# Optimization experiments

Measured on AMD Instinct MI355X. Metric: run time of the kernel, lower is better.

Reference implementation:

```python
import jax, jax.numpy as jnp
import numpy as np

TEMPERATURE = 32.0  # sqrt(d_model=1024)

def setup_inputs() -> dict:
    key = jax.random.key(0)
    kq, kk, kv = jax.random.split(key, 3)
    B, H, S, D = 2, 16, 2048, 64
    q = jax.random.normal(kq, (B, H, S, D), dtype=jnp.float32)
    k = jax.random.normal(kk, (B, H, S, D), dtype=jnp.float32)
    v = jax.random.normal(kv, (B, H, S, D), dtype=jnp.float32)
    mask = jnp.ones((B, 1, 1, S), dtype=jnp.int32)  # key-padding mask, 1 = keep
    return {"q": q, "k": k, "v": v, "mask": mask}

def reference(q, k, v, mask):
    # scores: [B,H,S,S]
    scores = jnp.einsum('bhqd,bhkd->bhqk', q / TEMPERATURE, k)
    scores = jnp.where(mask == 0, jnp.float32(-1e9), scores)
    attention = jax.nn.softmax(scores, axis=-1)
    # dropout is identity at inference (module's nn.Dropout in eval mode)
    output = jnp.einsum('bhqk,bhkd->bhqd', attention, v)
    return (output, attention)
```

## Files before the change

### kernel.cpp

```cpp
#include <hip/hip_runtime.h>
#include <hip/hip_bf16.h>


#define S_LEN 2048
#define D_DIM 64
#define BM 64
#define BN 64
#define NT (S_LEN / BN)
#define LDP 72
#define PSTR 136
#define BH_N 32

typedef __attribute__((ext_vector_type(8))) short bf16x8;
typedef __attribute__((ext_vector_type(4))) float f32x4;

__device__ __forceinline__ unsigned pack_bf16(float a, float b) {
    union { __hip_bfloat162 h; unsigned u; } cv;
    cv.h = __float22bfloat162_rn(make_float2(a, b));
    return cv.u;
}
__device__ __forceinline__ unsigned short bf1(float x) {
    union { __hip_bfloat16 h; unsigned short u; } cv;
    cv.h = __float2bfloat16(x);
    return cv.u;
}
__device__ __forceinline__ float bf2f(unsigned bits) {
    return __uint_as_float(bits);
}

__global__ __launch_bounds__(256)
void conv_k(const float* __restrict__ Kg, unsigned short* __restrict__ Kw) {
    size_t i = (size_t)(blockIdx.x * 256 + threadIdx.x) * 8;
    const float4 v0 = *(const float4*)(Kg + i);
    const float4 v1 = *(const float4*)(Kg + i + 4);
    uint4 o;
    o.x = pack_bf16(v0.x, v0.y);
    o.y = pack_bf16(v0.z, v0.w);
    o.z = pack_bf16(v1.x, v1.y);
    o.w = pack_bf16(v1.z, v1.w);
    *(uint4*)(Kw + i) = o;
}

__global__ __launch_bounds__(256)
void conv_vt(const float* __restrict__ Vg, unsigned short* __restrict__ Vtw) {
    const int bh = blockIdx.y;
    const int d  = threadIdx.x & 63;
    const int kq = threadIdx.x >> 6;
    const int key0 = blockIdx.x * 32 + kq * 8;
    const float* Vb = Vg + ((size_t)bh * S_LEN + key0) * D_DIM + d;
    float f[8];
    #pragma unroll
    for (int i = 0; i < 8; ++i) f[i] = Vb[i * D_DIM];
    uint4 o;
    o.x = pack_bf16(f[0], f[1]);
    o.y = pack_bf16(f[2], f[3]);
    o.z = pack_bf16(f[4], f[5]);
    o.w = pack_bf16(f[6], f[7]);
    *(uint4*)(Vtw + ((size_t)bh * D_DIM + d) * S_LEN + key0) = o;
}

template <int PRE>
__global__ __launch_bounds__(256, 4)
void attn_kernel(const float* __restrict__ Qg, const float* __restrict__ Kg,
                 const float* __restrict__ Vg, const int* __restrict__ Mg,
                 const unsigned short* __restrict__ Kw,
                 const unsigned short* __restrict__ Vtw,
                 float* __restrict__ Og, float* __restrict__ Ag) {
    __shared__ unsigned short Ks[BN * LDP];
    __shared__ unsigned short QV[D_DIM * LDP];
    __shared__ unsigned short Pb[BM * PSTR];
    __shared__ int maskS[BN];

    const int tid  = threadIdx.x;
    const int w    = tid >> 6;
    const int lane = tid & 63;
    const int l15  = lane & 15;
    const int quad = lane >> 4;

    const int qt = blockIdx.x;
    const int bh = blockIdx.y;
    const int b  = bh >> 4;
    const int q0 = qt * BM;
    const int qrow = w * 16 + l15;

    const float* Qb = Qg + ((size_t)bh * S_LEN + q0) * D_DIM;
    const int*   Mb = Mg + (size_t)b * S_LEN;
    float* Ob = Og + ((size_t)bh * S_LEN + q0) * D_DIM;
    float* Ab = Ag + ((size_t)bh * S_LEN + q0) * (size_t)S_LEN;

    {
        const float sc = 0.04508422f;
        #pragma unroll
        for (int i = 0; i < 4; ++i) {
            int f = tid + i * 256;
            int row = f >> 4, c4 = f & 15;
            const float4 v = *(const float4*)(Qb + row * D_DIM + c4 * 4);
            *(uint2*)(&QV[row * LDP + c4 * 4]) =
                make_uint2(pack_bf16(v.x * sc, v.y * sc), pack_bf16(v.z * sc, v.w * sc));
        }
    }
    __syncthreads();

    bf16x8 aq[2];
    #pragma unroll
    for (int ks = 0; ks < 2; ++ks)
        aq[ks] = *(const bf16x8*)(&QV[qrow * LDP + ks * 32 + quad * 8]);

    auto stage_k = [&](int key0) {
        if constexpr (PRE) {
            const unsigned short* Kt = Kw + (size_t)bh * S_LEN * D_DIM + (size_t)key0 * D_DIM;
            #pragma unroll
            for (int i = 0; i < 2; ++i) {
                int idx = tid + i * 256;
                int row = idx >> 3, c = idx & 7;
                uint4 vv = *(const uint4*)(Kt + row * D_DIM + c * 8);
                *(uint4*)(&Ks[row * LDP + c * 8]) = vv;
            }
        } else {
            const float* Kb = Kg + ((size_t)bh * S_LEN + key0) * D_DIM;
            #pragma unroll
            for (int i = 0; i < 4; ++i) {
                int f = tid + i * 256;
                int row = f >> 4, c4 = f & 15;
                const float4 v = *(const float4*)(Kb + row * D_DIM + c4 * 4);
                *(uint2*)(&Ks[row * LDP + c4 * 4]) =
                    make_uint2(pack_bf16(v.x, v.y), pack_bf16(v.z, v.w));
            }
        }
    };
    auto stage_v = [&](int key0) {
        if constexpr (PRE) {
            const unsigned short* Vt = Vtw + (size_t)bh * D_DIM * S_LEN + key0;
            #pragma unroll
            for (int i = 0; i < 2; ++i) {
                int idx = tid + i * 256;
                int d = idx >> 3, c = idx & 7;
                uint4 vv = *(const uint4*)(Vt + (size_t)d * S_LEN + c * 8);
                *(uint4*)(&QV[d * LDP + c * 8]) = vv;
            }
        } else {
            int key = tid & 63, g = tid >> 6;
            #pragma unroll
            for (int i = 0; i < 4; ++i) {
                int d0 = (g * 4 + i) * 4;
                const float4 v = *(const float4*)(Vg + ((size_t)bh * S_LEN + key0 + key) * D_DIM + d0);
                QV[(d0 + 0) * LDP + key] = bf1(v.x);
                QV[(d0 + 1) * LDP + key] = bf1(v.y);
                QV[(d0 + 2) * LDP + key] = bf1(v.z);
                QV[(d0 + 3) * LDP + key] = bf1(v.w);
            }
        }
    };

    float lsum = 0.f;

    for (int kt = 0; kt < NT; ++kt) {
        const int key0 = kt * BN;
        stage_k(key0);
        if (tid < BN) maskS[tid] = Mb[key0 + tid];
        __syncthreads();

        #pragma unroll
        for (int cb = 0; cb < 4; ++cb) {
            f32x4 acc = {0.f, 0.f, 0.f, 0.f};
            #pragma unroll
            for (int ks = 0; ks < 2; ++ks) {
                bf16x8 bk = *(const bf16x8*)(&Ks[(cb * 16 + l15) * LDP + ks * 32 + quad * 8]);
                acc = __builtin_amdgcn_mfma_f32_16x16x32_bf16(bk, aq[ks], acc, 0, 0, 0);
            }
            const int4 m4 = *(const int4*)(&maskS[cb * 16 + quad * 4]);
            float e0 = m4.x ? __builtin_exp2f(acc[0]) : 0.f;
            float e1 = m4.y ? __builtin_exp2f(acc[1]) : 0.f;
            float e2 = m4.z ? __builtin_exp2f(acc[2]) : 0.f;
            float e3 = m4.w ? __builtin_exp2f(acc[3]) : 0.f;
            lsum += (e0 + e1) + (e2 + e3);
        }
        __syncthreads();
    }

    lsum += __shfl_xor(lsum, 16);
    lsum += __shfl_xor(lsum, 32);
    const float linv = 1.0f / lsum;

    f32x4 oacc[4];
    #pragma unroll
    for (int db = 0; db < 4; ++db) oacc[db] = (f32x4){0.f, 0.f, 0.f, 0.f};

    for (int kt2 = 0; kt2 < NT / 2; ++kt2) {
        #pragma unroll
        for (int half = 0; half < 2; ++half) {
            const int key0 = (kt2 * 2 + half) * BN;
            stage_k(key0);
            stage_v(key0);
            if (tid < BN) maskS[tid] = Mb[key0 + tid];
            __syncthreads();

            #pragma unroll
            for (int cb = 0; cb < 4; ++cb) {
                f32x4 acc = {0.f, 0.f, 0.f, 0.f};
                #pragma unroll
                for (int ks = 0; ks < 2; ++ks) {
                    bf16x8 bk = *(const bf16x8*)(&Ks[(cb * 16 + l15) * LDP + ks * 32 + quad * 8]);
                    acc = __builtin_amdgcn_mfma_f32_16x16x32_bf16(bk, aq[ks], acc, 0, 0, 0);
                }
                const int4 m4 = *(const int4*)(&maskS[cb * 16 + quad * 4]);
                float p0 = (m4.x ? __builtin_exp2f(acc[0]) : 0.f) * linv;
                float p1 = (m4.y ? __builtin_exp2f(acc[1]) : 0.f) * linv;
                float p2 = (m4.z ? __builtin_exp2f(acc[2]) : 0.f) * linv;
                float p3 = (m4.w ? __builtin_exp2f(acc[3]) : 0.f) * linv;
                *(uint2*)(&Pb[qrow * PSTR + half * 64 + cb * 16 + quad * 4]) =
                    make_uint2(pack_bf16(p0, p1), pack_bf16(p2, p3));
            }

            #pragma unroll
            for (int ks2 = 0; ks2 < 2; ++ks2) {
                bf16x8 ap = *(const bf16x8*)(&Pb[qrow * PSTR + half * 64 + ks2 * 32 + quad * 8]);
                #pragma unroll
                for (int db = 0; db < 4; ++db) {
                    bf16x8 bv = *(const bf16x8*)(&QV[(db * 16 + l15) * LDP + ks2 * 32 + quad * 8]);
                    oacc[db] = __builtin_amdgcn_mfma_f32_16x16x32_bf16(bv, ap, oacc[db], 0, 0, 0);
                }
            }
            __syncthreads();
        }

        const int key00 = kt2 * 2 * BN;
        #pragma unroll
        for (int i = 0; i < 8; ++i) {
            int idx = tid + i * 256;
            int row = idx >> 5, c4 = idx & 31;
            uint2 pu = *(const uint2*)(&Pb[row * PSTR + c4 * 4]);
            f32x4 t;
            t[0] = bf2f(pu.x << 16); t[1] = bf2f(pu.x & 0xffff0000u);
            t[2] = bf2f(pu.y << 16); t[3] = bf2f(pu.y & 0xffff0000u);
            __builtin_nontemporal_store(
                t, (f32x4*)(Ab + (size_t)row * S_LEN + key00 + c4 * 4));
        }
    }

    #pragma unroll
    for (int db = 0; db < 4; ++db) {
        f32x4 o4 = oacc[db];
        __builtin_nontemporal_store(
            o4, (f32x4*)(Ob + (size_t)qrow * D_DIM + db * 16 + quad * 4));
    }
}

extern "C" void kernel_launch(void* const* d_in, const int* in_sizes, int n_in,
                              void* d_out, int out_size, void* d_ws, size_t ws_size,
                              hipStream_t stream) {
    const float* q = (const float*)d_in[0];
    const float* k = (const float*)d_in[1];
    const float* v = (const float*)d_in[2];
    const int* mask = (const int*)d_in[3];
    float* out = (float*)d_out;
    float* attn = out + (size_t)2 * 16 * 2048 * 64;

    const size_t kw_elems = (size_t)BH_N * S_LEN * D_DIM;
    const size_t need = 2 * kw_elems * sizeof(unsigned short);
    dim3 block(256);
    dim3 grid(S_LEN / BM, BH_N);

    if (d_ws && ws_size >= need) {
        unsigned short* Kw  = (unsigned short*)d_ws;
        unsigned short* Vtw = Kw + kw_elems;
        conv_k<<<dim3((unsigned)(kw_elems / 8 / 256)), block, 0, stream>>>(k, Kw);
        conv_vt<<<dim3(S_LEN / 32, BH_N), block, 0, stream>>>(v, Vtw);
        attn_kernel<1><<<grid, block, 0, stream>>>(q, k, v, mask, Kw, Vtw, out, attn);
    } else {
        attn_kernel<0><<<grid, block, 0, stream>>>(q, k, v, mask, nullptr, nullptr, out, attn);
    }
}
```

Measured before the change: 636.8 us.

## Split softmax row-sum pass into a separate LDS-free kernel

Moves the first pass, which computes softmax denominators, out of the attention kernel into its own kernel. That kernel reads bf16 K directly from global memory, with no shared-memory staging or barriers, and writes the per-row sums to workspace. The main kernel then loads the precomputed inverse sum and does only the second pass. The aim is to drop the barrier-heavy LDS staging from the first pass; the cost is an extra launch, a small workspace buffer and uncoalesced-style global K reads.

```diff
diff --git a/kernel.cpp b/kernel.cpp
--- a/kernel.cpp
+++ b/kernel.cpp
@@ -59,12 +59,75 @@
     *(uint4*)(Vtw + ((size_t)bh * D_DIM + d) * S_LEN + key0) = o;
 }
 
-template <int PRE>
+__global__ __launch_bounds__(256, 4)
+void lsum_kernel(const float* __restrict__ Qg, const int* __restrict__ Mg,
+                 const unsigned short* __restrict__ Kw, float* __restrict__ Ls) {
+    const int tid  = threadIdx.x;
+    const int w    = tid >> 6;
+    const int lane = tid & 63;
+    const int l15  = lane & 15;
+    const int quad = lane >> 4;
+
+    const int qt = blockIdx.x;
+    const int bh = blockIdx.y;
+    const int b  = bh >> 4;
+    const int q0 = qt * BM;
+    const int qrow = w * 16 + l15;
+
+    const float* Qb = Qg + ((size_t)bh * S_LEN + q0) * D_DIM;
+    const int*   Mb = Mg + (size_t)b * S_LEN;
+    const unsigned short* Kb = Kw + (size_t)bh * S_LEN * D_DIM;
+
+    bf16x8 aq[2];
+    {
+        const float sc = 0.04508422f;
+        #pragma unroll
+        for (int ks = 0; ks < 2; ++ks) {
+            const float* qp = Qb + qrow * D_DIM + ks * 32 + quad * 8;
+            const float4 a = *(const float4*)(qp);
+            const float4 c = *(const float4*)(qp + 4);
+            union { bf16x8 v; uint4 u; } cv;
+            cv.u.x = pack_bf16(a.x * sc, a.y * sc);
+            cv.u.y = pack_bf16(a.z * sc, a.w * sc);
+            cv.u.z = pack_bf16(c.x * sc, c.y * sc);
+            cv.u.w = pack_bf16(c.z * sc, c.w * sc);
+            aq[ks] = cv.v;
+        }
+    }
+
+    float lsum = 0.f;
+    for (int kt = 0; kt < NT; ++kt) {
+        const unsigned short* Kt = Kb + (size_t)kt * BN * D_DIM;
+        const int* Mt = Mb + kt * BN + quad * 4;
+        #pragma unroll
+        for (int cb = 0; cb < 4; ++cb) {
+            f32x4 acc = {0.f, 0.f, 0.f, 0.f};
+            #pragma unroll
+            for (int ks = 0; ks < 2; ++ks) {
+                bf16x8 bk = *(const bf16x8*)(Kt + (cb * 16 + l15) * D_DIM + ks * 32 + quad * 8);
+                acc = __builtin_amdgcn_mfma_f32_16x16x32_bf16(bk, aq[ks], acc, 0, 0, 0);
+            }
+            const int4 m4 = *(const int4*)(Mt + cb * 16);
+            float e0 = m4.x ? __builtin_exp2f(acc[0]) : 0.f;
+            float e1 = m4.y ? __builtin_exp2f(acc[1]) : 0.f;
+            float e2 = m4.z ? __builtin_exp2f(acc[2]) : 0.f;
+            float e3 = m4.w ? __builtin_exp2f(acc[3]) : 0.f;
+            lsum += (e0 + e1) + (e2 + e3);
+        }
+    }
+    lsum += __shfl_xor(lsum, 16);
+    lsum += __shfl_xor(lsum, 32);
+    if (quad == 0)
+        Ls[(size_t)bh * S_LEN + q0 + qrow] = lsum;
+}
+
+template <int PRE, int P1>
 __global__ __launch_bounds__(256, 4)
 void attn_kernel(const float* __restrict__ Qg, const float* __restrict__ Kg,
                  const float* __restrict__ Vg, const int* __restrict__ Mg,
                  const unsigned short* __restrict__ Kw,
                  const unsigned short* __restrict__ Vtw,
+                 const float* __restrict__ Ls,
                  float* __restrict__ Og, float* __restrict__ Ag) {
     __shared__ unsigned short Ks[BN * LDP];
     __shared__ unsigned short QV[D_DIM * LDP];
@@ -152,35 +215,38 @@
         }
     };
 
-    float lsum = 0.f;
-
-    for (int kt = 0; kt < NT; ++kt) {
-        const int key0 = kt * BN;
-        stage_k(key0);
-        if (tid < BN) maskS[tid] = Mb[key0 + tid];
+    float linv;
+    if constexpr (P1) {
+        float lsum = 0.f;
+        for (int kt = 0; kt < NT; ++kt) {
+            const int key0 = kt * BN;
+            stage_k(key0);
+            if (tid < BN) maskS[tid] = Mb[key0 + tid];
+            __syncthreads();
+            #pragma unroll
+            for (int cb = 0; cb < 4; ++cb) {
+                f32x4 acc = {0.f, 0.f, 0.f, 0.f};
+                #pragma unroll
+                for (int ks = 0; ks < 2; ++ks) {
+                    bf16x8 bk = *(const bf16x8*)(&Ks[(cb * 16 + l15) * LDP + ks * 32 + quad * 8]);
+                    acc = __builtin_amdgcn_mfma_f32_16x16x32_bf16(bk, aq[ks], acc, 0, 0, 0);
+                }
+                const int4 m4 = *(const int4*)(&maskS[cb * 16 + quad * 4]);
+                float e0 = m4.x ? __builtin_exp2f(acc[0]) : 0.f;
+                float e1 = m4.y ? __builtin_exp2f(acc[1]) : 0.f;
+                float e2 = m4.z ? __builtin_exp2f(acc[2]) : 0.f;
+                float e3 = m4.w ? __builtin_exp2f(acc[3]) : 0.f;
+                lsum += (e0 + e1) + (e2 + e3);
+            }
+            __syncthreads();
+        }
+        lsum += __shfl_xor(lsum, 16);
+        lsum += __shfl_xor(lsum, 32);
+        linv = 1.0f / lsum;
+    } else {
+        linv = 1.0f / Ls[(size_t)bh * S_LEN + q0 + qrow];
         __syncthreads();
-
-        #pragma unroll
-        for (int cb = 0; cb < 4; ++cb) {
-            f32x4 acc = {0.f, 0.f, 0.f, 0.f};
-            #pragma unroll
-            for (int ks = 0; ks < 2; ++ks) {
-                bf16x8 bk = *(const bf16x8*)(&Ks[(cb * 16 + l15) * LDP + ks * 32 + quad * 8]);
-                acc = __builtin_amdgcn_mfma_f32_16x16x32_bf16(bk, aq[ks], acc, 0, 0, 0);
-            }
-            const int4 m4 = *(const int4*)(&maskS[cb * 16 + quad * 4]);
-            float e0 = m4.x ? __builtin_exp2f(acc[0]) : 0.f;
-            float e1 = m4.y ? __builtin_exp2f(acc[1]) : 0.f;
-            float e2 = m4.z ? __builtin_exp2f(acc[2]) : 0.f;
-            float e3 = m4.w ? __builtin_exp2f(acc[3]) : 0.f;
-            lsum += (e0 + e1) + (e2 + e3);
-        }
-        __syncthreads();
-    }
-
-    lsum += __shfl_xor(lsum, 16);
-    lsum += __shfl_xor(lsum, 32);
-    const float linv = 1.0f / lsum;
+    }
 
     f32x4 oacc[4];
     #pragma unroll
@@ -257,17 +323,22 @@
     float* attn = out + (size_t)2 * 16 * 2048 * 64;
 
     const size_t kw_elems = (size_t)BH_N * S_LEN * D_DIM;
-    const size_t need = 2 * kw_elems * sizeof(unsigned short);
+    const size_t kv_bytes = 2 * kw_elems * sizeof(unsigned short);
+    const size_t ls_bytes = (size_t)BH_N * S_LEN * sizeof(float);
+    const size_t need = kv_bytes + ls_bytes;
     dim3 block(256);
     dim3 grid(S_LEN / BM, BH_N);
 
     if (d_ws && ws_size >= need) {
         unsigned short* Kw  = (unsigned short*)d_ws;
         unsigned short* Vtw = Kw + kw_elems;
+        float* Ls = (float*)((char*)d_ws + kv_bytes);
         conv_k<<<dim3((unsigned)(kw_elems / 8 / 256)), block, 0, stream>>>(k, Kw);
         conv_vt<<<dim3(S_LEN / 32, BH_N), block, 0, stream>>>(v, Vtw);
-        attn_kernel<1><<<grid, block, 0, stream>>>(q, k, v, mask, Kw, Vtw, out, attn);
+        lsum_kernel<<<grid, block, 0, stream>>>(q, mask, Kw, Ls);
+        attn_kernel<1, 0><<<grid, block, 0, stream>>>(q, k, v, mask, Kw, Vtw, Ls, out, attn);
     } else {
-        attn_kernel<0><<<grid, block, 0, stream>>>(q, k, v, mask, nullptr, nullptr, out, attn);
-    }
-}
+        attn_kernel<0, 1><<<grid, block, 0, stream>>>(q, k, v, mask, nullptr, nullptr,
+                                                      nullptr, out, attn);
+    }
+}
```

After: 721.8 us. 1.13x slower.

## Pre-swizzle K and V tiles into MFMA fragment order; read K directly in pass one

Applied to the files above, without the earlier changes.

The conversion kernels now write bf16 K and transposed V in a per-tile layout that matches the MFMA operand fragment order, so each lane's 8-element chunk is contiguous. The first (row-sum) pass drops LDS staging and both barriers, with each wave loading its K fragments and mask entries straight from global memory. The aim is to remove LDS traffic and synchronisation from the softmax-normaliser pass and to make global loads fully coalesced. The trade-off is that every wave re-reads the same K tile from global memory or cache instead of sharing one staged copy.

```diff
diff --git a/kernel.cpp b/kernel.cpp
--- a/kernel.cpp
+++ b/kernel.cpp
@@ -10,6 +10,7 @@
 #define LDP 72
 #define PSTR 136
 #define BH_N 32
+#define TILE_USH 4096
 
 typedef __attribute__((ext_vector_type(8))) short bf16x8;
 typedef __attribute__((ext_vector_type(4))) float f32x4;
@@ -30,15 +31,25 @@
 
 __global__ __launch_bounds__(256)
 void conv_k(const float* __restrict__ Kg, unsigned short* __restrict__ Kw) {
-    size_t i = (size_t)(blockIdx.x * 256 + threadIdx.x) * 8;
-    const float4 v0 = *(const float4*)(Kg + i);
-    const float4 v1 = *(const float4*)(Kg + i + 4);
-    uint4 o;
-    o.x = pack_bf16(v0.x, v0.y);
-    o.y = pack_bf16(v0.z, v0.w);
-    o.z = pack_bf16(v1.x, v1.y);
-    o.w = pack_bf16(v1.z, v1.w);
-    *(uint4*)(Kw + i) = o;
+    const int kt = blockIdx.x;
+    const int bh = blockIdx.y;
+    const int tid = threadIdx.x;
+    const float* Kb = Kg + ((size_t)bh * S_LEN + kt * 64) * D_DIM;
+    unsigned short* Ko = Kw + ((size_t)bh * NT + kt) * TILE_USH;
+    #pragma unroll
+    for (int i = 0; i < 2; ++i) {
+        int c = tid + i * 256;
+        int l15 = c & 15, quad = (c >> 4) & 3, ks = (c >> 6) & 1, cb = (c >> 7) & 3;
+        const float* src = Kb + (cb * 16 + l15) * D_DIM + ks * 32 + quad * 8;
+        const float4 a = *(const float4*)src;
+        const float4 b = *(const float4*)(src + 4);
+        uint4 o;
+        o.x = pack_bf16(a.x, a.y);
+        o.y = pack_bf16(a.z, a.w);
+        o.z = pack_bf16(b.x, b.y);
+        o.w = pack_bf16(b.z, b.w);
+        *(uint4*)(Ko + (size_t)c * 8) = o;
+    }
 }
 
 __global__ __launch_bounds__(256)
@@ -56,7 +67,12 @@
     o.y = pack_bf16(f[2], f[3]);
     o.z = pack_bf16(f[4], f[5]);
     o.w = pack_bf16(f[6], f[7]);
-    *(uint4*)(Vtw + ((size_t)bh * D_DIM + d) * S_LEN + key0) = o;
+    const int kt  = key0 >> 6;
+    const int ko  = key0 & 63;
+    const int ks2 = ko >> 5, quad = (ko >> 3) & 3;
+    const int db  = d >> 4,  l15  = d & 15;
+    const int c   = db * 128 + ks2 * 64 + quad * 16 + l15;
+    *(uint4*)(Vtw + ((size_t)bh * NT + kt) * TILE_USH + (size_t)c * 8) = o;
 }
 
 template <int PRE>
@@ -108,13 +124,13 @@
 
     auto stage_k = [&](int key0) {
         if constexpr (PRE) {
-            const unsigned short* Kt = Kw + (size_t)bh * S_LEN * D_DIM + (size_t)key0 * D_DIM;
+            const unsigned short* Kt = Kw + ((size_t)bh * NT + (key0 >> 6)) * TILE_USH;
             #pragma unroll
             for (int i = 0; i < 2; ++i) {
-                int idx = tid + i * 256;
-                int row = idx >> 3, c = idx & 7;
-                uint4 vv = *(const uint4*)(Kt + row * D_DIM + c * 8);
-                *(uint4*)(&Ks[row * LDP + c * 8]) = vv;
+                int c = tid + i * 256;
+                uint4 vv = *(const uint4*)(Kt + (size_t)c * 8);
+                int l15c = c & 15, quadc = (c >> 4) & 3, ksc = (c >> 6) & 1, cbc = (c >> 7) & 3;
+                *(uint4*)(&Ks[(cbc * 16 + l15c) * LDP + ksc * 32 + quadc * 8]) = vv;
             }
         } else {
             const float* Kb = Kg + ((size_t)bh * S_LEN + key0) * D_DIM;
@@ -130,19 +146,19 @@
     };
     auto stage_v = [&](int key0) {
         if constexpr (PRE) {
-            const unsigned short* Vt = Vtw + (size_t)bh * D_DIM * S_LEN + key0;
+            const unsigned short* Vt = Vtw + ((size_t)bh * NT + (key0 >> 6)) * TILE_USH;
             #pragma unroll
             for (int i = 0; i < 2; ++i) {
-                int idx = tid + i * 256;
-                int d = idx >> 3, c = idx & 7;
-                uint4 vv = *(const uint4*)(Vt + (size_t)d * S_LEN + c * 8);
-                *(uint4*)(&QV[d * LDP + c * 8]) = vv;
+                int c = tid + i * 256;
+                uint4 vv = *(const uint4*)(Vt + (size_t)c * 8);
+                int l15c = c & 15, quadc = (c >> 4) & 3, ks2c = (c >> 6) & 1, dbc = (c >> 7) & 3;
+                *(uint4*)(&QV[(dbc * 16 + l15c) * LDP + ks2c * 32 + quadc * 8]) = vv;
             }
         } else {
-            int key = tid & 63, g = tid >> 6;
+            int key = tid & 63, g2 = tid >> 6;
             #pragma unroll
             for (int i = 0; i < 4; ++i) {
-                int d0 = (g * 4 + i) * 4;
+                int d0 = (g2 * 4 + i) * 4;
                 const float4 v = *(const float4*)(Vg + ((size_t)bh * S_LEN + key0 + key) * D_DIM + d0);
                 QV[(d0 + 0) * LDP + key] = bf1(v.x);
                 QV[(d0 + 1) * LDP + key] = bf1(v.y);
@@ -154,33 +170,57 @@
 
     float lsum = 0.f;
 
-    for (int kt = 0; kt < NT; ++kt) {
-        const int key0 = kt * BN;
-        stage_k(key0);
-        if (tid < BN) maskS[tid] = Mb[key0 + tid];
-        __syncthreads();
-
-        #pragma unroll
-        for (int cb = 0; cb < 4; ++cb) {
-            f32x4 acc = {0.f, 0.f, 0.f, 0.f};
-            #pragma unroll
-            for (int ks = 0; ks < 2; ++ks) {
-                bf16x8 bk = *(const bf16x8*)(&Ks[(cb * 16 + l15) * LDP + ks * 32 + quad * 8]);
-                acc = __builtin_amdgcn_mfma_f32_16x16x32_bf16(bk, aq[ks], acc, 0, 0, 0);
-            }
-            const int4 m4 = *(const int4*)(&maskS[cb * 16 + quad * 4]);
-            float e0 = m4.x ? __builtin_exp2f(acc[0]) : 0.f;
-            float e1 = m4.y ? __builtin_exp2f(acc[1]) : 0.f;
-            float e2 = m4.z ? __builtin_exp2f(acc[2]) : 0.f;
-            float e3 = m4.w ? __builtin_exp2f(acc[3]) : 0.f;
-            lsum += (e0 + e1) + (e2 + e3);
-        }
-        __syncthreads();
+    if constexpr (PRE) {
+        const unsigned short* Kb = Kw + (size_t)bh * NT * TILE_USH;
+        for (int kt = 0; kt < NT; ++kt) {
+            const unsigned short* Kt = Kb + (size_t)kt * TILE_USH + lane * 8;
+            const int* Mt = Mb + kt * BN + quad * 4;
+            #pragma unroll
+            for (int cb = 0; cb < 4; ++cb) {
+                f32x4 acc = {0.f, 0.f, 0.f, 0.f};
+                #pragma unroll
+                for (int ks = 0; ks < 2; ++ks) {
+                    bf16x8 bk = *(const bf16x8*)(Kt + cb * 1024 + ks * 512);
+                    acc = __builtin_amdgcn_mfma_f32_16x16x32_bf16(bk, aq[ks], acc, 0, 0, 0);
+                }
+                const int4 m4 = *(const int4*)(Mt + cb * 16);
+                float e0 = m4.x ? __builtin_exp2f(acc[0]) : 0.f;
+                float e1 = m4.y ? __builtin_exp2f(acc[1]) : 0.f;
+                float e2 = m4.z ? __builtin_exp2f(acc[2]) : 0.f;
+                float e3 = m4.w ? __builtin_exp2f(acc[3]) : 0.f;
+                lsum += (e0 + e1) + (e2 + e3);
+            }
+        }
+    } else {
+        for (int kt = 0; kt < NT; ++kt) {
+            const int key0 = kt * BN;
+            stage_k(key0);
+            if (tid < BN) maskS[tid] = Mb[key0 + tid];
+            __syncthreads();
+            #pragma unroll
+            for (int cb = 0; cb < 4; ++cb) {
+                f32x4 acc = {0.f, 0.f, 0.f, 0.f};
+                #pragma unroll
+                for (int ks = 0; ks < 2; ++ks) {
+                    bf16x8 bk = *(const bf16x8*)(&Ks[(cb * 16 + l15) * LDP + ks * 32 + quad * 8]);
+                    acc = __builtin_amdgcn_mfma_f32_16x16x32_bf16(bk, aq[ks], acc, 0, 0, 0);
+                }
+                const int4 m4 = *(const int4*)(&maskS[cb * 16 + quad * 4]);
+                float e0 = m4.x ? __builtin_exp2f(acc[0]) : 0.f;
+                float e1 = m4.y ? __builtin_exp2f(acc[1]) : 0.f;
+                float e2 = m4.z ? __builtin_exp2f(acc[2]) : 0.f;
+                float e3 = m4.w ? __builtin_exp2f(acc[3]) : 0.f;
+                lsum += (e0 + e1) + (e2 + e3);
+            }
+            __syncthreads();
+        }
     }
 
     lsum += __shfl_xor(lsum, 16);
     lsum += __shfl_xor(lsum, 32);
     const float linv = 1.0f / lsum;
+
+    __syncthreads();
 
     f32x4 oacc[4];
     #pragma unroll
@@ -264,7 +304,7 @@
     if (d_ws && ws_size >= need) {
         unsigned short* Kw  = (unsigned short*)d_ws;
         unsigned short* Vtw = Kw + kw_elems;
-        conv_k<<<dim3((unsigned)(kw_elems / 8 / 256)), block, 0, stream>>>(k, Kw);
+        conv_k<<<dim3(NT, BH_N), block, 0, stream>>>(k, Kw);
         conv_vt<<<dim3(S_LEN / 32, BH_N), block, 0, stream>>>(v, Vtw);
         attn_kernel<1><<<grid, block, 0, stream>>>(q, k, v, mask, Kw, Vtw, out, attn);
     } else {
```

Result: no change. 628.1 us, median of 2 (-1.4%).
